# Optimization experiments

Measured on AMD Instinct MI355X. Metric: run time of the kernel, lower is better.

## Reference

```python
import jax, jax.numpy as jnp
import numpy as np

MLP_CHANNELS = 128
MLP_KERNEL = 5


def setup_inputs() -> dict:
    key = jax.random.key(0)
    k1, k2 = jax.random.split(key)
    b, c, h, w = 16, MLP_CHANNELS, 128, 128
    num_w = MLP_KERNEL ** 2 * c + c  # 3328
    inp = jax.random.normal(k1, (b, c, h, w), dtype=jnp.float32)
    # mimic ini_weights_ scaling: conv weights ~ N(0, 6/(k^2+c)), bias ~ N(0, 1/c)
    weights = jax.random.normal(k2, (b, num_w), dtype=jnp.float32)
    off = MLP_KERNEL ** 2 * c
    scale = jnp.concatenate([
        jnp.full((off,), np.sqrt(6.0 / (MLP_KERNEL ** 2 + c)), dtype=jnp.float32),
        jnp.full((c,), np.sqrt(1.0 / c), dtype=jnp.float32),
    ])
    weights = weights * scale[None, :]
    return {"input": inp, "weights": weights}


def reference(input, weights):
    b, c, h, w = input.shape
    k = MLP_KERNEL
    off = k * k * c
    # per-sample depthwise filters [b, c, 1, k, k] and biases [b, c]
    wk = weights[:, :off].reshape(b, c, 1, k, k)
    bias = weights[:, off:off + c]

    def dwconv(x, wt):
        # x: [c,h,w], wt: [c,1,k,k]; depthwise conv via feature_group_count=c
        return jax.lax.conv_general_dilated(
            x[None], wt, window_strides=(1, 1), padding='SAME',
            dimension_numbers=('NCHW', 'OIHW', 'NCHW'),
            feature_group_count=c)[0]

    out = jax.vmap(dwconv)(input, wk)          # [b,c,h,w]
    out = out + bias[:, :, None, None]          # fused bias
    return jax.nn.silu(out)                     # act
```

## Files before the change

kernel.cpp:

```cpp
#include <hip/hip_runtime.h>
#include <math.h>

#define C_CH 128
#define HW 128
#define KK 5
#define PAD 2
#define TILE_ROWS 64
#define LDS_ROWS (TILE_ROWS + 2*PAD)
#define LDS_COLS (HW + 2*PAD)
#define NW (KK*KK*C_CH + C_CH)

__global__ __launch_bounds__(256, 4) void hyperconv_dw_silu(
    const float* __restrict__ inp, const float* __restrict__ wts,
    float* __restrict__ out)
{
    __shared__ float s[LDS_ROWS][LDS_COLS];

    const int tid  = threadIdx.x;
    const int tile = blockIdx.x;
    const int c    = blockIdx.y;
    const int b    = blockIdx.z;

    const float* wt = wts + (size_t)b * NW;
    float wk[25];
    #pragma unroll
    for (int j = 0; j < 25; ++j) wk[j] = wt[c * 25 + j];
    const float bias = wt[KK*KK*C_CH + c];

    const int row0 = tile * TILE_ROWS;
    const float* plane = inp + ((size_t)(b * C_CH + c)) * (HW * HW);

    for (int i = tid; i < LDS_ROWS * 4; i += 256) {
        int r  = i >> 2;
        int ci = i & 3;
        int col = (ci < 2) ? ci : (HW + ci);
        s[r][col] = 0.0f;
    }

    for (int idx = tid; idx < LDS_ROWS * (HW / 4); idx += 256) {
        int r  = idx >> 5;
        int cs = idx & 31;
        int gr = row0 - PAD + r;
        float4 v = make_float4(0.f, 0.f, 0.f, 0.f);
        if (gr >= 0 && gr < HW) {
            v = *(const float4*)(plane + (size_t)gr * HW + cs * 4);
        }
        float2* dst = (float2*)&s[r][2 + cs * 4];
        dst[0] = make_float2(v.x, v.y);
        dst[1] = make_float2(v.z, v.w);
    }
    __syncthreads();

    const int colg = tid & 31;
    const int rowg = tid >> 5;
    float* oplane = out + ((size_t)(b * C_CH + c)) * (HW * HW);

    #pragma unroll
    for (int p = 0; p < 2; ++p) {
        const int ro = p * 32 + rowg * 4;

        float acc[4][4];
        #pragma unroll
        for (int i = 0; i < 4; ++i)
            #pragma unroll
            for (int j = 0; j < 4; ++j)
                acc[i][j] = bias;

        #pragma unroll
        for (int r = 0; r < 8; ++r) {
            const float4 a  = *(const float4*)&s[ro + r][colg * 4];
            const float4 bb = *(const float4*)&s[ro + r][colg * 4 + 4];
            float x[8] = {a.x, a.y, a.z, a.w, bb.x, bb.y, bb.z, bb.w};

            #pragma unroll
            for (int orow = 0; orow < 4; ++orow) {
                const int kh = r - orow;
                if (kh < 0 || kh > 4) continue;
                #pragma unroll
                for (int oc = 0; oc < 4; ++oc) {
                    #pragma unroll
                    for (int kw = 0; kw < 5; ++kw) {
                        acc[orow][oc] = fmaf(wk[kh * 5 + kw], x[oc + kw], acc[orow][oc]);
                    }
                }
            }
        }

        #pragma unroll
        for (int orow = 0; orow < 4; ++orow) {
            float4 o;
            float v0 = acc[orow][0], v1 = acc[orow][1], v2 = acc[orow][2], v3 = acc[orow][3];
            o.x = v0 / (1.0f + expf(-v0));
            o.y = v1 / (1.0f + expf(-v1));
            o.z = v2 / (1.0f + expf(-v2));
            o.w = v3 / (1.0f + expf(-v3));
            *(float4*)(oplane + (size_t)(row0 + ro + orow) * HW + colg * 4) = o;
        }
    }
}

extern "C" void kernel_launch(void* const* d_in, const int* in_sizes, int n_in,
                              void* d_out, int out_size, void* d_ws, size_t ws_size,
                              hipStream_t stream) {
    const float* inp = (const float*)d_in[0];
    const float* wts = (const float*)d_in[1];
    float* out = (float*)d_out;

    const int batch = in_sizes[1] / NW;
    dim3 grid(HW / TILE_ROWS, C_CH, batch);
    hyperconv_dw_silu<<<grid, 256, 0, stream>>>(inp, wts, out);
}
```

Baseline: 238.5 us.

## Replace LDS tiling with register-rotating row strips reading global directly

Drops the shared-memory tile and the __syncthreads. Each thread now streams 20 input rows straight from global memory into registers and uses a 5-slot rotating accumulator ring to produce 16 output rows per thread. One block handles a whole channel plane, and launch bounds are raised for occupancy. SiLU now uses the hardware exp2 and rcp intrinsics instead of expf and a divide, which trades a little accuracy for fewer instructions. The risk is that overlapping float2 global loads across threads and rows lean on the cache instead of LDS reuse, and the grid has fewer blocks.

```diff
diff --git a/kernel.cpp b/kernel.cpp
--- a/kernel.cpp
+++ b/kernel.cpp
@@ -1,100 +1,78 @@
 #include <hip/hip_runtime.h>
-#include <math.h>
 
 #define C_CH 128
 #define HW 128
-#define KK 5
-#define PAD 2
-#define TILE_ROWS 64
-#define LDS_ROWS (TILE_ROWS + 2*PAD)
-#define LDS_COLS (HW + 2*PAD)
-#define NW (KK*KK*C_CH + C_CH)
+#define NW (25 * C_CH + C_CH)
 
-__global__ __launch_bounds__(256, 4) void hyperconv_dw_silu(
+__global__ __launch_bounds__(256, 8) void hyperconv_dw_silu(
     const float* __restrict__ inp, const float* __restrict__ wts,
     float* __restrict__ out)
 {
-    __shared__ float s[LDS_ROWS][LDS_COLS];
+    const int tid   = threadIdx.x;
+    const int colg  = tid & 31;
+    const int strip = tid >> 5;
+    const int c     = blockIdx.x;
+    const int b     = blockIdx.y;
 
-    const int tid  = threadIdx.x;
-    const int tile = blockIdx.x;
-    const int c    = blockIdx.y;
-    const int b    = blockIdx.z;
-
-    const float* wt = wts + (size_t)b * NW;
+    const float* wt = wts + (size_t)b * NW + c * 25;
     float wk[25];
     #pragma unroll
-    for (int j = 0; j < 25; ++j) wk[j] = wt[c * 25 + j];
-    const float bias = wt[KK*KK*C_CH + c];
+    for (int j = 0; j < 25; ++j) wk[j] = wt[j];
+    const float bias = wts[(size_t)b * NW + 25 * C_CH + c];
 
-    const int row0 = tile * TILE_ROWS;
-    const float* plane = inp + ((size_t)(b * C_CH + c)) * (HW * HW);
+    const float* plane  = inp + ((size_t)(b * C_CH + c)) * (HW * HW);
+    float*       oplane = out + ((size_t)(b * C_CH + c)) * (HW * HW);
 
-    for (int i = tid; i < LDS_ROWS * 4; i += 256) {
-        int r  = i >> 2;
-        int ci = i & 3;
-        int col = (ci < 2) ? ci : (HW + ci);
-        s[r][col] = 0.0f;
-    }
+    const int R0 = strip * 16;
+    const int j0 = colg * 4;
 
-    for (int idx = tid; idx < LDS_ROWS * (HW / 4); idx += 256) {
-        int r  = idx >> 5;
-        int cs = idx & 31;
-        int gr = row0 - PAD + r;
-        float4 v = make_float4(0.f, 0.f, 0.f, 0.f);
-        if (gr >= 0 && gr < HW) {
-            v = *(const float4*)(plane + (size_t)gr * HW + cs * 4);
-        }
-        float2* dst = (float2*)&s[r][2 + cs * 4];
-        dst[0] = make_float2(v.x, v.y);
-        dst[1] = make_float2(v.z, v.w);
-    }
-    __syncthreads();
+    float acc[5][4];
+    #pragma unroll
+    for (int s = 0; s < 5; ++s)
+        #pragma unroll
+        for (int oc = 0; oc < 4; ++oc) acc[s][oc] = bias;
 
-    const int colg = tid & 31;
-    const int rowg = tid >> 5;
-    float* oplane = out + ((size_t)(b * C_CH + c)) * (HW * HW);
+    const bool haveL = (colg > 0);
+    const bool haveR = (colg < 31);
 
     #pragma unroll
-    for (int p = 0; p < 2; ++p) {
-        const int ro = p * 32 + rowg * 4;
+    for (int ir = 0; ir < 20; ++ir) {
+        const int gr = R0 - 2 + ir;
+        const bool vr = (unsigned)gr < (unsigned)HW;
+        const float* rp = plane + (size_t)(vr ? gr : 0) * HW + j0;
 
-        float acc[4][4];
-        #pragma unroll
-        for (int i = 0; i < 4; ++i)
-            #pragma unroll
-            for (int j = 0; j < 4; ++j)
-                acc[i][j] = bias;
+        float2 A  = (vr && haveL) ? *(const float2*)(rp - 2) : make_float2(0.f, 0.f);
+        float2 Bq = vr            ? *(const float2*)(rp    ) : make_float2(0.f, 0.f);
+        float2 Cq = vr            ? *(const float2*)(rp + 2) : make_float2(0.f, 0.f);
+        float2 D  = (vr && haveR) ? *(const float2*)(rp + 4) : make_float2(0.f, 0.f);
+        float x[8] = {A.x, A.y, Bq.x, Bq.y, Cq.x, Cq.y, D.x, D.y};
 
         #pragma unroll
-        for (int r = 0; r < 8; ++r) {
-            const float4 a  = *(const float4*)&s[ro + r][colg * 4];
-            const float4 bb = *(const float4*)&s[ro + r][colg * 4 + 4];
-            float x[8] = {a.x, a.y, a.z, a.w, bb.x, bb.y, bb.z, bb.w};
-
+        for (int kh = 0; kh < 5; ++kh) {
+            const int k = ir - kh;
+            if (k < 0 || k > 15) continue;
+            const int s = k % 5;
             #pragma unroll
-            for (int orow = 0; orow < 4; ++orow) {
-                const int kh = r - orow;
-                if (kh < 0 || kh > 4) continue;
+            for (int oc = 0; oc < 4; ++oc)
                 #pragma unroll
-                for (int oc = 0; oc < 4; ++oc) {
-                    #pragma unroll
-                    for (int kw = 0; kw < 5; ++kw) {
-                        acc[orow][oc] = fmaf(wk[kh * 5 + kw], x[oc + kw], acc[orow][oc]);
-                    }
-                }
-            }
+                for (int kw = 0; kw < 5; ++kw)
+                    acc[s][oc] = fmaf(wk[kh * 5 + kw], x[oc + kw], acc[s][oc]);
         }
 
-        #pragma unroll
-        for (int orow = 0; orow < 4; ++orow) {
+        if (ir >= 4) {
+            const int k = ir - 4;
+            const int s = k % 5;
             float4 o;
-            float v0 = acc[orow][0], v1 = acc[orow][1], v2 = acc[orow][2], v3 = acc[orow][3];
-            o.x = v0 / (1.0f + expf(-v0));
-            o.y = v1 / (1.0f + expf(-v1));
-            o.z = v2 / (1.0f + expf(-v2));
-            o.w = v3 / (1.0f + expf(-v3));
-            *(float4*)(oplane + (size_t)(row0 + ro + orow) * HW + colg * 4) = o;
+            float* po = (float*)&o;
+            #pragma unroll
+            for (int oc = 0; oc < 4; ++oc) {
+                const float v = acc[s][oc];
+                const float t = __builtin_amdgcn_exp2f(v * -1.44269504088896341f);
+                po[oc] = v * __builtin_amdgcn_rcpf(1.0f + t);
+            }
+            *(float4*)(oplane + (size_t)(R0 + k) * HW + j0) = o;
+            #pragma unroll
+            for (int oc = 0; oc < 4; ++oc) acc[s][oc] = bias;
         }
     }
 }
@@ -107,6 +85,6 @@
     float* out = (float*)d_out;
 
     const int batch = in_sizes[1] / NW;
-    dim3 grid(HW / TILE_ROWS, C_CH, batch);
+    dim3 grid(C_CH, batch);
     hyperconv_dw_silu<<<grid, 256, 0, stream>>>(inp, wts, out);
 }
```

After: 299.9 us. 1.26x slower.
